# Kernel optimization log

Measured on AMD Instinct MI355X. Metric: run time of the kernel, lower is better.

Reference implementation:

```python
import jax, jax.numpy as jnp
import numpy as np

B, N, IN_F, OUT_F, H = 4, 2048, 128, 128, 4
D = OUT_F // H  # head_dim = 32
NEG_SLOPE = 0.2


def setup_inputs() -> dict:
    key = jax.random.key(0)
    k1, k2, k3, k4, k5 = jax.random.split(key, 5)
    x = jax.random.normal(k1, (B, N, IN_F), dtype=jnp.float32)
    adj = jax.random.randint(k2, (N, N), 0, 2, dtype=jnp.int32)
    adj = adj.at[jnp.arange(N), jnp.arange(N)].set(1)  # self-loops
    # xavier-uniform-like init
    lim_w = float(np.sqrt(6.0 / (IN_F + OUT_F)))
    W = jax.random.uniform(k3, (OUT_F, IN_F), minval=-lim_w, maxval=lim_w, dtype=jnp.float32)
    lim_a = float(np.sqrt(6.0 / (H + D)))
    a_src = jax.random.uniform(k4, (H, D), minval=-lim_a, maxval=lim_a, dtype=jnp.float32)
    a_dst = jax.random.uniform(k5, (H, D), minval=-lim_a, maxval=lim_a, dtype=jnp.float32)
    return {"x": x, "adj": adj, "W": W, "a_src": a_src, "a_dst": a_dst}


def reference(x, adj, W, a_src, a_dst):
    Bx, Nx, _ = x.shape
    # linear projection: (B,N,out) -> (B,N,H,D)
    h = jnp.einsum('bni,oi->bno', x, W).reshape(Bx, Nx, H, D)
    e_src = jnp.einsum('bnhd,hd->bnh', h, a_src)  # (B,N,H)
    e_dst = jnp.einsum('bnhd,hd->bnh', h, a_dst)  # (B,N,H)
    # scores: (B,N_src,H,N_dst)
    scores = jax.nn.leaky_relu(
        e_src[:, :, :, None] + e_dst.transpose(0, 2, 1)[:, None, :, :],
        negative_slope=NEG_SLOPE,
    )
    mask = adj[None, :, None, :]  # (1,N,1,N)
    scores = jnp.where(mask == 0, -jnp.inf, scores)
    attn = jax.nn.softmax(scores, axis=-1)  # (B,N,H,N); dropout is identity at eval
    out = jnp.einsum('bnhm,bmhd->bnhd', attn, h)  # (B,N,H,D)
    return out.reshape(Bx, Nx, H * D)
```

## Files before the change

kernel.cpp:

```cpp
#include <hip/hip_runtime.h>
#include <math.h>

#define BB 4
#define NN 2048
#define FF 128
#define HH 4
#define DD 32
#define NEG_SLOPE 0.2f
#define LOG2E 1.4426950408889634f

typedef __attribute__((ext_vector_type(8))) short short8;
typedef __attribute__((ext_vector_type(4))) float floatx4;

__device__ __forceinline__ float exp2_fast(float x) {
#if __has_builtin(__builtin_amdgcn_exp2f)
    return __builtin_amdgcn_exp2f(x);
#else
    return exp2f(x);
#endif
}

__device__ __forceinline__ unsigned short to_bf16(float f) {
    unsigned int ui = __float_as_uint(f);
    ui += 0x7FFFu + ((ui >> 16) & 1u);
    return (unsigned short)(ui >> 16);
}

__global__ __launch_bounds__(256) void k_pack_adj(const int* __restrict__ adj,
                                                  unsigned int* __restrict__ bits) {
    int idx = blockIdx.x * 256 + threadIdx.x;
    int n = idx >> 6, w = idx & 63;
    const int4* base = (const int4*)(adj + (size_t)n * NN + w * 32);
    unsigned int word = 0;
#pragma unroll
    for (int q = 0; q < 8; ++q) {
        int4 a = base[q];
        word |= ((unsigned int)(a.x & 1)) << (q * 4 + 0);
        word |= ((unsigned int)(a.y & 1)) << (q * 4 + 1);
        word |= ((unsigned int)(a.z & 1)) << (q * 4 + 2);
        word |= ((unsigned int)(a.w & 1)) << (q * 4 + 3);
    }
    bits[idx] = word;
}

__global__ __launch_bounds__(256) void k_gemm_fused(const float* __restrict__ x,
                                                    const float* __restrict__ W,
                                                    const float* __restrict__ a_src,
                                                    const float* __restrict__ a_dst,
                                                    unsigned short* __restrict__ ht,
                                                    float* __restrict__ es_t,
                                                    float* __restrict__ ed_t) {
    __shared__ float xs[16][FF];
    __shared__ float wt[32][132];
    __shared__ float as_s[FF], ad_s[FF];
    __shared__ unsigned short tile2[16][136];
    int t = threadIdx.x;
    long rows0 = (long)blockIdx.x * 16;
    if (t < FF) { as_s[t] = a_src[t]; ad_s[t] = a_dst[t]; }
#pragma unroll
    for (int k = 0; k < 2; ++k) {
        int q = t + k * 256;
        int r = q >> 5, c4 = q & 31;
        float4 v = ((const float4*)(x + (rows0 + r) * FF))[c4];
        *(float4*)&xs[r][c4 * 4] = v;
    }
    int og = t & 31, rg = t >> 5;
    float acc[2][4];
#pragma unroll
    for (int a = 0; a < 2; ++a)
#pragma unroll
        for (int c = 0; c < 4; ++c) acc[a][c] = 0.f;

    int wo = t & 127, wg = t >> 7;
    for (int i0 = 0; i0 < FF; i0 += 32) {
        __syncthreads();
#pragma unroll
        for (int u = 0; u < 4; ++u) {
            float4 v = *(const float4*)(W + (long)wo * FF + i0 + wg * 16 + u * 4);
            wt[wg * 16 + u * 4 + 0][wo] = v.x;
            wt[wg * 16 + u * 4 + 1][wo] = v.y;
            wt[wg * 16 + u * 4 + 2][wo] = v.z;
            wt[wg * 16 + u * 4 + 3][wo] = v.w;
        }
        __syncthreads();
#pragma unroll
        for (int i = 0; i < 32; ++i) {
            float4 w4 = *(const float4*)&wt[i][og * 4];
            float x0 = xs[rg * 2 + 0][i0 + i];
            float x1 = xs[rg * 2 + 1][i0 + i];
            acc[0][0] += x0 * w4.x; acc[0][1] += x0 * w4.y;
            acc[0][2] += x0 * w4.z; acc[0][3] += x0 * w4.w;
            acc[1][0] += x1 * w4.x; acc[1][1] += x1 * w4.y;
            acc[1][2] += x1 * w4.z; acc[1][3] += x1 * w4.w;
        }
    }

    int head = og >> 3;
    int b = (int)(rows0 >> 11);
    int m_block = (int)(rows0 & 2047);
    float es0 = 0.f, ed0 = 0.f, es1 = 0.f, ed1 = 0.f;
#pragma unroll
    for (int c = 0; c < 4; ++c) {
        int col = og * 4 + c;
        es0 += acc[0][c] * as_s[col]; ed0 += acc[0][c] * ad_s[col];
        es1 += acc[1][c] * as_s[col]; ed1 += acc[1][c] * ad_s[col];
    }
#pragma unroll
    for (int k = 1; k < 8; k <<= 1) {
        es0 += __shfl_xor(es0, k); ed0 += __shfl_xor(ed0, k);
        es1 += __shfl_xor(es1, k); ed1 += __shfl_xor(ed1, k);
    }
    if ((og & 7) == 0) {
        size_t eb = (size_t)(b * HH + head) * NN + m_block + rg * 2;
        es_t[eb]     = es0 * LOG2E; ed_t[eb]     = ed0 * LOG2E;
        es_t[eb + 1] = es1 * LOG2E; ed_t[eb + 1] = ed1 * LOG2E;
    }

#pragma unroll
    for (int a = 0; a < 2; ++a)
#pragma unroll
        for (int c = 0; c < 4; ++c)
            tile2[rg * 2 + a][og * 4 + c] = to_bf16(acc[a][c]);
    __syncthreads();
    {
        int cg = t >> 1, half = t & 1;
        int d = cg & 31, hd = cg >> 5;
        unsigned short tmp[8];
#pragma unroll
        for (int j = 0; j < 8; ++j) tmp[j] = tile2[half * 8 + j][cg];
        unsigned short* op = ht + ((size_t)(b * HH + hd) * DD + d) * NN + m_block + half * 8;
        *(int4*)op = *(const int4*)tmp;
    }
}

#define HB_HALF 1024
__global__ __launch_bounds__(512) void k_attn(
        const unsigned short* __restrict__ ht,
        const unsigned int* __restrict__ bits,
        const float* __restrict__ es_t,
        const float* __restrict__ ed_t,
        float* __restrict__ out) {
    __shared__ unsigned short hb[DD * HB_HALF];
    __shared__ float eds[NN];
    __shared__ unsigned int bitw[128][68];
    int t = threadIdx.x;
    int n0 = blockIdx.x * 128;
    int bh = blockIdx.y;
    int b = bh >> 2, head = bh & 3;

    ((float4*)eds)[t] = ((const float4*)(ed_t + (size_t)bh * NN))[t];
#pragma unroll
    for (int k = 0; k < 4; ++k) {
        int q = t + k * 512;
        int nl = q >> 4, wq = q & 15;
        int4 v = ((const int4*)(bits + (size_t)(n0 + nl) * 64))[wq];
        *(int4*)&bitw[nl][wq * 4] = v;
    }

    int wid = t >> 6, lane = t & 63;
    int q = lane >> 4, r = lane & 15;
    int qo = q * 8, sw = r & 7;
    int n_l = wid * 16 + r;
    float es = es_t[(size_t)bh * NN + n0 + n_l];
    const unsigned short* htp = ht + (size_t)bh * DD * NN;

    floatx4 acc0 = {0.f, 0.f, 0.f, 0.f};
    floatx4 acc1 = {0.f, 0.f, 0.f, 0.f};
    floatx4 accd = {0.f, 0.f, 0.f, 0.f};
    union { short8 s8; int i[4]; } ones;
    ones.i[0] = 0x3F803F80; ones.i[1] = 0x3F803F80;
    ones.i[2] = 0x3F803F80; ones.i[3] = 0x3F803F80;

    for (int half = 0; half < 2; ++half) {
        __syncthreads();
#pragma unroll
        for (int k = 0; k < 8; ++k) {
            int qq = t + k * 512;
            int d = qq >> 7, cm = qq & 127;
            int4 v = *(const int4*)(htp + (size_t)d * NN + half * HB_HALF + cm * 8);
            *(int4*)&hb[d * HB_HALF + ((cm ^ (d & 7)) * 8)] = v;
        }
        __syncthreads();
        const unsigned int* brow = bitw[n_l];
#pragma unroll 2
        for (int m0 = 0; m0 < HB_HALF; m0 += 32) {
            int mg = half * HB_HALF + m0;
            unsigned int word = brow[mg >> 5];
            float4 e0 = *(const float4*)&eds[mg + qo];
            float4 e1 = *(const float4*)&eds[mg + qo + 4];
            float w[8];
#pragma unroll
            for (int j = 0; j < 8; ++j) {
                float ev = j < 4 ? (&e0.x)[j] : (&e1.x)[j - 4];
                float s = es + ev;
                float l = fmaxf(s, NEG_SLOPE * s);
                float v = exp2_fast(l);
                w[j] = (word & (1u << (qo + j))) ? v : 0.f;
            }
            union { short8 s8; int i[4]; } af;
#pragma unroll
            for (int p = 0; p < 4; ++p)
                af.i[p] = __builtin_amdgcn_perm(__float_as_uint(w[2 * p + 1]),
                                                __float_as_uint(w[2 * p]),
                                                0x07060302u);
            int cs = ((m0 + qo) >> 3) ^ sw;
            short8 b0 = *(const short8*)&hb[r * HB_HALF + cs * 8];
            short8 b1 = *(const short8*)&hb[(16 + r) * HB_HALF + cs * 8];
            acc0 = __builtin_amdgcn_mfma_f32_16x16x32_bf16(af.s8, b0, acc0, 0, 0, 0);
            acc1 = __builtin_amdgcn_mfma_f32_16x16x32_bf16(af.s8, b1, acc1, 0, 0, 0);
            accd = __builtin_amdgcn_mfma_f32_16x16x32_bf16(af.s8, ones.s8, accd, 0, 0, 0);
        }
    }

#pragma unroll
    for (int reg = 0; reg < 4; ++reg) {
        int nrow = n0 + wid * 16 + q * 4 + reg;
        float inv = 1.0f / accd[reg];
        float* op = out + ((size_t)(b * NN + nrow)) * FF + head * DD;
        op[r]      = acc0[reg] * inv;
        op[16 + r] = acc1[reg] * inv;
    }
}

extern "C" void kernel_launch(void* const* d_in, const int* in_sizes, int n_in,
                              void* d_out, int out_size, void* d_ws, size_t ws_size,
                              hipStream_t stream) {
    const float* x     = (const float*)d_in[0];
    const int*   adj   = (const int*)d_in[1];
    const float* W     = (const float*)d_in[2];
    const float* a_src = (const float*)d_in[3];
    const float* a_dst = (const float*)d_in[4];
    float* out = (float*)d_out;

    float* es_t = (float*)d_ws;
    float* ed_t = es_t + (size_t)BB * HH * NN;
    unsigned int* bits = (unsigned int*)(ed_t + (size_t)BB * HH * NN);
    unsigned short* ht = (unsigned short*)(bits + (size_t)NN * (NN / 32));

    hipLaunchKernelGGL(k_pack_adj, dim3(NN * (NN / 32) / 256), dim3(256), 0, stream,
                       adj, bits);
    hipLaunchKernelGGL(k_gemm_fused, dim3(BB * NN / 16), dim3(256), 0, stream,
                       x, W, a_src, a_dst, ht, es_t, ed_t);
    hipLaunchKernelGGL(k_attn, dim3(NN / 128, BB * HH), dim3(512), 0, stream,
                       ht, bits, es_t, ed_t, out);
}
```

Baseline: 106.3 us.

## Merge prep kernels and split attention key range across 16 waves with reduction

The adjacency bit-packing and the projection GEMM now run as one launch, with blocks past index 512 doing the packing. The attention kernel moves to 1024 threads: the whole bf16 h tile for the (batch, head) is loaded into shared memory once with padded rows instead of an XOR swizzle. Each half of the waves handles half of the key range, with adjacency bits held in registers. Partial accumulators are then combined through shared memory before normalisation. This removes one launch, the mid-loop reload barrier and the bit staging in shared memory, at the cost of larger shared-memory use, more register pressure and an extra reduction step.

```diff
diff --git a/kernel.cpp b/kernel.cpp
--- a/kernel.cpp
+++ b/kernel.cpp
@@ -26,35 +26,38 @@
     return (unsigned short)(ui >> 16);
 }
 
-__global__ __launch_bounds__(256) void k_pack_adj(const int* __restrict__ adj,
-                                                  unsigned int* __restrict__ bits) {
-    int idx = blockIdx.x * 256 + threadIdx.x;
-    int n = idx >> 6, w = idx & 63;
-    const int4* base = (const int4*)(adj + (size_t)n * NN + w * 32);
-    unsigned int word = 0;
-#pragma unroll
-    for (int q = 0; q < 8; ++q) {
-        int4 a = base[q];
-        word |= ((unsigned int)(a.x & 1)) << (q * 4 + 0);
-        word |= ((unsigned int)(a.y & 1)) << (q * 4 + 1);
-        word |= ((unsigned int)(a.z & 1)) << (q * 4 + 2);
-        word |= ((unsigned int)(a.w & 1)) << (q * 4 + 3);
-    }
-    bits[idx] = word;
-}
-
-__global__ __launch_bounds__(256) void k_gemm_fused(const float* __restrict__ x,
-                                                    const float* __restrict__ W,
-                                                    const float* __restrict__ a_src,
-                                                    const float* __restrict__ a_dst,
-                                                    unsigned short* __restrict__ ht,
-                                                    float* __restrict__ es_t,
-                                                    float* __restrict__ ed_t) {
+__global__ __launch_bounds__(256) void k_prep(const float* __restrict__ x,
+                                              const float* __restrict__ W,
+                                              const float* __restrict__ a_src,
+                                              const float* __restrict__ a_dst,
+                                              const int* __restrict__ adj,
+                                              unsigned short* __restrict__ ht,
+                                              float* __restrict__ es_t,
+                                              float* __restrict__ ed_t,
+                                              unsigned int* __restrict__ bits) {
     __shared__ float xs[16][FF];
     __shared__ float wt[32][132];
     __shared__ float as_s[FF], ad_s[FF];
     __shared__ unsigned short tile2[16][136];
     int t = threadIdx.x;
+
+    if (blockIdx.x >= 512) {
+        int idx = (blockIdx.x - 512) * 256 + t;
+        int n = idx >> 6, w = idx & 63;
+        const int4* base = (const int4*)(adj + (size_t)n * NN + w * 32);
+        unsigned int word = 0;
+#pragma unroll
+        for (int q = 0; q < 8; ++q) {
+            int4 a = base[q];
+            word |= ((unsigned int)(a.x & 1)) << (q * 4 + 0);
+            word |= ((unsigned int)(a.y & 1)) << (q * 4 + 1);
+            word |= ((unsigned int)(a.z & 1)) << (q * 4 + 2);
+            word |= ((unsigned int)(a.w & 1)) << (q * 4 + 3);
+        }
+        bits[idx] = word;
+        return;
+    }
+
     long rows0 = (long)blockIdx.x * 16;
     if (t < FF) { as_s[t] = a_src[t]; ad_s[t] = a_dst[t]; }
 #pragma unroll
@@ -133,36 +136,46 @@
     }
 }
 
-#define HB_HALF 1024
-__global__ __launch_bounds__(512) void k_attn(
+#define HTS 2056
+__global__ __launch_bounds__(1024, 4) void k_attn(
         const unsigned short* __restrict__ ht,
         const unsigned int* __restrict__ bits,
         const float* __restrict__ es_t,
         const float* __restrict__ ed_t,
         float* __restrict__ out) {
-    __shared__ unsigned short hb[DD * HB_HALF];
+    __shared__ unsigned short hb[DD * HTS];
     __shared__ float eds[NN];
-    __shared__ unsigned int bitw[128][68];
     int t = threadIdx.x;
     int n0 = blockIdx.x * 128;
     int bh = blockIdx.y;
     int b = bh >> 2, head = bh & 3;
 
-    ((float4*)eds)[t] = ((const float4*)(ed_t + (size_t)bh * NN))[t];
-#pragma unroll
-    for (int k = 0; k < 4; ++k) {
-        int q = t + k * 512;
-        int nl = q >> 4, wq = q & 15;
-        int4 v = ((const int4*)(bits + (size_t)(n0 + nl) * 64))[wq];
-        *(int4*)&bitw[nl][wq * 4] = v;
-    }
-
     int wid = t >> 6, lane = t & 63;
     int q = lane >> 4, r = lane & 15;
-    int qo = q * 8, sw = r & 7;
-    int n_l = wid * 16 + r;
+    int qo = q * 8;
+    int half = wid >> 3, wsub = wid & 7;
+    int n_l = wsub * 16 + r;
+
+    if (t < 512)
+        ((float4*)eds)[t] = ((const float4*)(ed_t + (size_t)bh * NN))[t];
+    {
+        const unsigned short* htp = ht + (size_t)bh * DD * NN;
+#pragma unroll
+        for (int k = 0; k < 8; ++k) {
+            int qq = t + k * 1024;
+            int d = qq >> 8, cm = qq & 255;
+            int4 v = *(const int4*)(htp + (size_t)d * NN + cm * 8);
+            *(int4*)&hb[d * HTS + cm * 8] = v;
+        }
+    }
+    int4 bw[8];
+    {
+        const int4* bp = (const int4*)(bits + (size_t)(n0 + n_l) * 64 + half * 32);
+#pragma unroll
+        for (int g = 0; g < 8; ++g) bw[g] = bp[g];
+    }
     float es = es_t[(size_t)bh * NN + n0 + n_l];
-    const unsigned short* htp = ht + (size_t)bh * DD * NN;
+    __syncthreads();
 
     floatx4 acc0 = {0.f, 0.f, 0.f, 0.f};
     floatx4 acc1 = {0.f, 0.f, 0.f, 0.f};
@@ -171,23 +184,19 @@
     ones.i[0] = 0x3F803F80; ones.i[1] = 0x3F803F80;
     ones.i[2] = 0x3F803F80; ones.i[3] = 0x3F803F80;
 
-    for (int half = 0; half < 2; ++half) {
-        __syncthreads();
-#pragma unroll
-        for (int k = 0; k < 8; ++k) {
-            int qq = t + k * 512;
-            int d = qq >> 7, cm = qq & 127;
-            int4 v = *(const int4*)(htp + (size_t)d * NN + half * HB_HALF + cm * 8);
-            *(int4*)&hb[d * HB_HALF + ((cm ^ (d & 7)) * 8)] = v;
-        }
-        __syncthreads();
-        const unsigned int* brow = bitw[n_l];
-#pragma unroll 2
-        for (int m0 = 0; m0 < HB_HALF; m0 += 32) {
-            int mg = half * HB_HALF + m0;
-            unsigned int word = brow[mg >> 5];
-            float4 e0 = *(const float4*)&eds[mg + qo];
-            float4 e1 = *(const float4*)&eds[mg + qo + 4];
+    const float* edh = eds + half * 1024;
+    const unsigned short* hrow0 = &hb[r * HTS + half * 1024 + qo];
+    const unsigned short* hrow1 = hrow0 + 16 * HTS;
+
+#pragma unroll
+    for (int g = 0; g < 8; ++g) {
+#pragma unroll
+        for (int c = 0; c < 4; ++c) {
+            unsigned int word = (unsigned int)((&bw[g].x)[c]);
+            int mb = (g * 4 + c) * 32;
+            unsigned int wq = word >> qo;
+            float4 e0 = *(const float4*)&edh[mb + qo];
+            float4 e1 = *(const float4*)&edh[mb + qo + 4];
             float w[8];
 #pragma unroll
             for (int j = 0; j < 8; ++j) {
@@ -195,7 +204,7 @@
                 float s = es + ev;
                 float l = fmaxf(s, NEG_SLOPE * s);
                 float v = exp2_fast(l);
-                w[j] = (word & (1u << (qo + j))) ? v : 0.f;
+                w[j] = (wq & (1u << j)) ? v : 0.f;
             }
             union { short8 s8; int i[4]; } af;
 #pragma unroll
@@ -203,22 +212,40 @@
                 af.i[p] = __builtin_amdgcn_perm(__float_as_uint(w[2 * p + 1]),
                                                 __float_as_uint(w[2 * p]),
                                                 0x07060302u);
-            int cs = ((m0 + qo) >> 3) ^ sw;
-            short8 b0 = *(const short8*)&hb[r * HB_HALF + cs * 8];
-            short8 b1 = *(const short8*)&hb[(16 + r) * HB_HALF + cs * 8];
+            short8 b0 = *(const short8*)(hrow0 + mb);
+            short8 b1 = *(const short8*)(hrow1 + mb);
             acc0 = __builtin_amdgcn_mfma_f32_16x16x32_bf16(af.s8, b0, acc0, 0, 0, 0);
             acc1 = __builtin_amdgcn_mfma_f32_16x16x32_bf16(af.s8, b1, acc1, 0, 0, 0);
             accd = __builtin_amdgcn_mfma_f32_16x16x32_bf16(af.s8, ones.s8, accd, 0, 0, 0);
         }
     }
 
-#pragma unroll
-    for (int reg = 0; reg < 4; ++reg) {
-        int nrow = n0 + wid * 16 + q * 4 + reg;
-        float inv = 1.0f / accd[reg];
-        float* op = out + ((size_t)(b * NN + nrow)) * FF + head * DD;
-        op[r]      = acc0[reg] * inv;
-        op[16 + r] = acc1[reg] * inv;
+    __syncthreads();
+    float* scr = (float*)hb;
+    if (wid >= 8) {
+        int base = ((wid - 8) * 64 + lane) * 12;
+        *(floatx4*)&scr[base + 0] = acc0;
+        *(floatx4*)&scr[base + 4] = acc1;
+        *(floatx4*)&scr[base + 8] = accd;
+    }
+    __syncthreads();
+    if (wid < 8) {
+        int base = (wid * 64 + lane) * 12;
+        floatx4 p0 = *(const floatx4*)&scr[base + 0];
+        floatx4 p1 = *(const floatx4*)&scr[base + 4];
+        floatx4 pd = *(const floatx4*)&scr[base + 8];
+#pragma unroll
+        for (int k = 0; k < 4; ++k) {
+            acc0[k] += p0[k]; acc1[k] += p1[k]; accd[k] += pd[k];
+        }
+#pragma unroll
+        for (int reg = 0; reg < 4; ++reg) {
+            int nrow = n0 + wsub * 16 + q * 4 + reg;
+            float inv = 1.0f / accd[reg];
+            float* op = out + ((size_t)(b * NN + nrow)) * FF + head * DD;
+            op[r]      = acc0[reg] * inv;
+            op[16 + r] = acc1[reg] * inv;
+        }
     }
 }
 
@@ -237,10 +264,8 @@
     unsigned int* bits = (unsigned int*)(ed_t + (size_t)BB * HH * NN);
     unsigned short* ht = (unsigned short*)(bits + (size_t)NN * (NN / 32));
 
-    hipLaunchKernelGGL(k_pack_adj, dim3(NN * (NN / 32) / 256), dim3(256), 0, stream,
-                       adj, bits);
-    hipLaunchKernelGGL(k_gemm_fused, dim3(BB * NN / 16), dim3(256), 0, stream,
-                       x, W, a_src, a_dst, ht, es_t, ed_t);
-    hipLaunchKernelGGL(k_attn, dim3(NN / 128, BB * HH), dim3(512), 0, stream,
+    hipLaunchKernelGGL(k_prep, dim3(1024), dim3(256), 0, stream,
+                       x, W, a_src, a_dst, adj, ht, es_t, ed_t, bits);
+    hipLaunchKernelGGL(k_attn, dim3(NN / 128, BB * HH), dim3(1024), 0, stream,
                        ht, bits, es_t, ed_t, out);
 }
```

Result: no change. 104.6 us (-1.6%).
